# Kernel tuning notes

Hardware: AMD Instinct MI355X
Metric: run time of the kernel (lower is better)

Reference implementation:

```python
import jax, jax.numpy as jnp
import numpy as np

D_MODEL = 512
N_HEADS = 8


def setup_inputs() -> dict:
    key = jax.random.key(0)
    ks = jax.random.split(key, 16)
    bs, S, D = 16, 512, D_MODEL
    def lin(k, fo, fi):
        lim = np.sqrt(6.0 / (fi + fo)).astype(np.float32)
        return jax.random.uniform(k, (fo, fi), jnp.float32, -lim, lim)
    inp = {
        'q': jax.random.normal(ks[0], (bs, S, D), jnp.float32),
        'k': jax.random.normal(ks[1], (bs, S, D), jnp.float32),
        'v': jax.random.normal(ks[2], (bs, S, D), jnp.float32),
        'sgap': jax.random.randint(ks[3], (bs, S), 0, 100, jnp.int64) if jax.config.jax_enable_x64 else jax.random.randint(ks[3], (bs, S), 0, 100, jnp.int32),
        'pcount': jax.random.randint(ks[4], (bs, S), 0, 50, jnp.int32),
        'Wq': lin(ks[5], D, D), 'bq': jnp.zeros((D,), jnp.float32),
        'Wk': lin(ks[6], D, D), 'bk': jnp.zeros((D,), jnp.float32),
        'Wv': lin(ks[7], D, D), 'bv': jnp.zeros((D,), jnp.float32),
        'Wo': lin(ks[8], D, D), 'bo': jnp.zeros((D,), jnp.float32),
        'gammas': jax.random.normal(ks[9], (N_HEADS, 1, 1), jnp.float32) * 0.5,
        'ln_g': jnp.ones((D,), jnp.float32), 'ln_b': jnp.zeros((D,), jnp.float32),
        'Wi1': lin(ks[10], D // 4, 2), 'bi1': jnp.zeros((D // 4,), jnp.float32),
        'Wi2': lin(ks[11], D, D // 4), 'bi2': jnp.zeros((D,), jnp.float32),
        'iscale': jnp.array([0.5], jnp.float32),
    }
    return inp


def reference(q, k, v, sgap, pcount, Wq, bq, Wk, bk, Wv, bv, Wo, bo, gammas, ln_g, ln_b, Wi1, bi1, Wi2, bi2, iscale):
    bs, S, D = q.shape
    h = gammas.shape[0]
    d_k = D // h
    def split_heads(x, W, b):
        return (x @ W.T + b).reshape(bs, S, h, d_k).transpose(0, 2, 1, 3)  # [b,h,S,d]
    qh = split_heads(q, Wq, bq)
    kh = split_heads(k, Wk, bk)
    vh = split_heads(v, Wv, bv)

    scores = jnp.einsum('bhid,bhjd->bhij', qh, kh) / jnp.sqrt(jnp.float32(d_k))
    # strict-causal mask (triu(ones,k=0)==0): attend only to j < i
    mask = jnp.tril(jnp.ones((S, S), bool), k=-1)[None, None]
    NEG = jnp.float32(-1e32)

    # no-grad temporal distance term
    p = jax.nn.softmax(jnp.where(mask, scores, NEG), axis=-1) * mask
    distcum = jnp.cumsum(p, axis=-1)
    disttotal = jnp.sum(p, axis=-1, keepdims=True)
    idx = jnp.arange(S, dtype=jnp.float32)
    pos = jnp.abs(idx[None, :] - idx[:, None])[None, None]
    dist = jax.lax.stop_gradient(jnp.sqrt(jnp.clip((disttotal - distcum) * pos, 0.0, None)))

    gam = -jax.nn.softplus(gammas)[None]  # [1,h,1,1]
    temporal = jnp.clip(jnp.exp(dist * gam), 1e-5, 1e5)
    attn = jax.nn.softmax(jnp.where(mask, scores * temporal, NEG), axis=-1)
    attn = attn.at[:, :, 0, :].set(0.0)  # zero_pad first query position

    X = jnp.einsum('bhij,bhjd->bhid', attn, vh).transpose(0, 2, 1, 3).reshape(bs, S, D)

    # InterferenceAddNorm
    def norm01(x):
        x = x.astype(jnp.float32)
        std = jnp.std(x, ddof=1) + 1e-6
        return (jnp.tanh((x - jnp.mean(x)) / std) + 1.0) / 2.0
    ii = jnp.stack([norm01(sgap), norm01(pcount)], axis=-1)  # [b,S,2]
    feat = jax.nn.relu(ii @ Wi1.T + bi1) @ Wi2.T + bi2
    Y = X + iscale * feat
    mu = jnp.mean(Y, -1, keepdims=True)
    var = jnp.var(Y, -1, keepdims=True)
    Yn = (Y - mu) / jnp.sqrt(var + 1e-5) * ln_g + ln_b
    return Yn @ Wo.T + bo
```

## Files before the change

kernel.cpp:

```cpp
#include <hip/hip_runtime.h>
#include <hip/hip_bf16.h>
#include <math.h>

typedef __attribute__((ext_vector_type(8))) short bf16x8;
typedef __attribute__((ext_vector_type(4))) float f32x4;
typedef __fp16 __attribute__((ext_vector_type(2))) h16x2;

__device__ __forceinline__ f32x4 mfma16(bf16x8 a, bf16x8 b, f32x4 c) {
  return __builtin_amdgcn_mfma_f32_16x16x32_bf16(a, b, c, 0, 0, 0);
}

__device__ __forceinline__ float scan16(float x) {
  int v;
  v = __builtin_amdgcn_update_dpp(0, __float_as_int(x), 0x111, 0xf, 0xf, true);
  x += __int_as_float(v);
  v = __builtin_amdgcn_update_dpp(0, __float_as_int(x), 0x112, 0xf, 0xf, true);
  x += __int_as_float(v);
  v = __builtin_amdgcn_update_dpp(0, __float_as_int(x), 0x114, 0xf, 0xf, true);
  x += __int_as_float(v);
  v = __builtin_amdgcn_update_dpp(0, __float_as_int(x), 0x118, 0xf, 0xf, true);
  x += __int_as_float(v);
  return x;
}

__global__ void stats_kernel(const int* __restrict__ sgap,
                             const int* __restrict__ pcount,
                             float* __restrict__ stats) {
  const int N = 16 * 512;
  long long s0 = 0, q0 = 0, s1 = 0, q1 = 0;
  for (int i = threadIdx.x; i < N; i += 256) {
    long long a = sgap[i];
    long long b = pcount[i];
    s0 += a; q0 += a * a;
    s1 += b; q1 += b * b;
  }
#pragma unroll
  for (int m = 32; m >= 1; m >>= 1) {
    s0 += __shfl_xor(s0, m, 64); q0 += __shfl_xor(q0, m, 64);
    s1 += __shfl_xor(s1, m, 64); q1 += __shfl_xor(q1, m, 64);
  }
  __shared__ long long red[4][4];
  const int w = threadIdx.x >> 6;
  if ((threadIdx.x & 63) == 0) {
    red[w][0] = s0; red[w][1] = q0; red[w][2] = s1; red[w][3] = q1;
  }
  __syncthreads();
  if (threadIdx.x == 0) {
    long long S0 = 0, Q0 = 0, S1 = 0, Q1 = 0;
    for (int i = 0; i < 4; ++i) {
      S0 += red[i][0]; Q0 += red[i][1]; S1 += red[i][2]; Q1 += red[i][3];
    }
    const double n = (double)N;
    const double mean0 = S0 / n, mean1 = S1 / n;
    const double var0 = ((double)Q0 - (double)S0 * (double)S0 / n) / (n - 1.0);
    const double var1 = ((double)Q1 - (double)S1 * (double)S1 / n) / (n - 1.0);
    const float std0 = (float)sqrt(var0) + 1e-6f;
    const float std1 = (float)sqrt(var1) + 1e-6f;
    stats[0] = (float)mean0; stats[1] = 1.0f / std0;
    stats[2] = (float)mean1; stats[3] = 1.0f / std1;
  }
}

template <int AMODE>
__device__ __forceinline__ void gemm_body(const void* __restrict__ Ain,
                                          const float* __restrict__ W,
                                          const float* __restrict__ bias,
                                          void* __restrict__ Out, const int omode) {
  constexpr int LDK = 40;
  __shared__ __hip_bfloat16 As[128 * LDK];
  __shared__ __hip_bfloat16 Bs[128 * LDK];
  const int tid = threadIdx.x;
  const int tm = blockIdx.x * 128;
  const int tn = blockIdx.y * 128;
  const int lane = tid & 63;
  const int wid = tid >> 6;
  const int wm = (wid >> 1) * 64;
  const int wn = (wid & 1) * 64;
  const int g = lane >> 4, l15 = lane & 15;

  const f32x4 Z = {0.f, 0.f, 0.f, 0.f};
  f32x4 acc[4][4];
#pragma unroll
  for (int m = 0; m < 4; ++m)
#pragma unroll
    for (int n = 0; n < 4; ++n) acc[m][n] = Z;

  for (int k0 = 0; k0 < 512; k0 += 32) {
#pragma unroll
    for (int p = 0; p < 4; ++p) {
      const int c = p * 256 + tid;
      const int row = c >> 3;
      const int kc = (c & 7) * 4;
      union { __hip_bfloat16 h[4]; uint2 u; } ua, ub;
      if (AMODE == 0) {
        const float4 x = *(const float4*)((const float*)Ain + (size_t)(tm + row) * 512 + k0 + kc);
        ua.h[0] = __float2bfloat16(x.x); ua.h[1] = __float2bfloat16(x.y);
        ua.h[2] = __float2bfloat16(x.z); ua.h[3] = __float2bfloat16(x.w);
      } else {
        ua.u = *(const uint2*)((const __hip_bfloat16*)Ain + (size_t)(tm + row) * 512 + k0 + kc);
      }
      const float4 wv = *(const float4*)(W + (size_t)(tn + row) * 512 + k0 + kc);
      ub.h[0] = __float2bfloat16(wv.x); ub.h[1] = __float2bfloat16(wv.y);
      ub.h[2] = __float2bfloat16(wv.z); ub.h[3] = __float2bfloat16(wv.w);
      *(uint2*)&As[row * LDK + kc] = ua.u;
      *(uint2*)&Bs[row * LDK + kc] = ub.u;
    }
    __syncthreads();
    bf16x8 af[4], bfv[4];
#pragma unroll
    for (int m = 0; m < 4; ++m)
      af[m] = *(const bf16x8*)&As[(wm + m * 16 + l15) * LDK + g * 8];
#pragma unroll
    for (int n = 0; n < 4; ++n)
      bfv[n] = *(const bf16x8*)&Bs[(wn + n * 16 + l15) * LDK + g * 8];
#pragma unroll
    for (int m = 0; m < 4; ++m)
#pragma unroll
      for (int n = 0; n < 4; ++n)
        acc[m][n] = mfma16(af[m], bfv[n], acc[m][n]);
    __syncthreads();
  }

#pragma unroll
  for (int n = 0; n < 4; ++n) {
    const int cc = tn + wn + n * 16 + l15;
    const float bv = bias[cc];
#pragma unroll
    for (int m = 0; m < 4; ++m) {
#pragma unroll
      for (int jj = 0; jj < 4; ++jj) {
        const int r = tm + wm + m * 16 + g * 4 + jj;
        const float v = acc[m][n][jj] + bv;
        if (omode == 2) {
          ((float*)Out)[(size_t)r * 512 + cc] = v;
        } else {
          const int bb = r >> 9, srow = r & 511, hh = cc >> 6, dd = cc & 63;
          if (omode == 0)
            ((__hip_bfloat16*)Out)[(((size_t)(bb * 8 + hh)) * 512 + srow) * 64 + dd] =
                __float2bfloat16(v);
          else
            ((__hip_bfloat16*)Out)[(((size_t)(bb * 8 + hh)) * 64 + dd) * 512 + srow] =
                __float2bfloat16(v);
        }
      }
    }
  }
}

__global__ __launch_bounds__(256) void gemm_qkv(
    const float* __restrict__ q, const float* __restrict__ k,
    const float* __restrict__ v, const float* __restrict__ Wq,
    const float* __restrict__ bq, const float* __restrict__ Wk,
    const float* __restrict__ bk, const float* __restrict__ Wv,
    const float* __restrict__ bv, __hip_bfloat16* __restrict__ qh,
    __hip_bfloat16* __restrict__ kh, __hip_bfloat16* __restrict__ vhT) {
  const int z = blockIdx.z;
  const float* A = (z == 0) ? q : (z == 1) ? k : v;
  const float* W = (z == 0) ? Wq : (z == 1) ? Wk : Wv;
  const float* bias = (z == 0) ? bq : (z == 1) ? bk : bv;
  void* Out = (z == 0) ? (void*)qh : (z == 1) ? (void*)kh : (void*)vhT;
  gemm_body<0>(A, W, bias, Out, (z == 2) ? 1 : 0);
}

__global__ __launch_bounds__(256) void gemm_wo(const __hip_bfloat16* __restrict__ Yn,
                                               const float* __restrict__ Wo,
                                               const float* __restrict__ bo,
                                               float* __restrict__ Out) {
  gemm_body<1>(Yn, Wo, bo, Out, 2);
}

#define PLD 40

__device__ __forceinline__ void attn_unit(
    const __hip_bfloat16* __restrict__ Q, const __hip_bfloat16* __restrict__ K,
    const __hip_bfloat16* __restrict__ V, __hip_bfloat16* __restrict__ Xb,
    __hip_bfloat16* Pw, const int i0, const int ntile, const float gam,
    const int b, const int h, const int lane) {
  const int g = lane >> 4, l15 = lane & 15;
  const float scale = 0.125f;
  const f32x4 Z = {0.f, 0.f, 0.f, 0.f};

  const bf16x8 qf0 = *(const bf16x8*)&Q[(i0 + l15) * 64 + g * 8];
  const bf16x8 qf1 = *(const bf16x8*)&Q[(i0 + l15) * 64 + 32 + g * 8];

  h16x2 sp[64];
  float d1p[4] = {0.f, 0.f, 0.f, 0.f};
#pragma unroll
  for (int t = 0; t < 32; ++t) {
    if (t < ntile) {
      const bf16x8 kf0 = *(const bf16x8*)&K[(t * 16 + l15) * 64 + g * 8];
      const bf16x8 kf1 = *(const bf16x8*)&K[(t * 16 + l15) * 64 + 32 + g * 8];
      f32x4 s = mfma16(qf0, kf0, Z);
      s = mfma16(qf1, kf1, s);
      sp[2 * t] = __builtin_amdgcn_cvt_pkrtz(s[0] * scale, s[1] * scale);
      sp[2 * t + 1] = __builtin_amdgcn_cvt_pkrtz(s[2] * scale, s[3] * scale);
      const int j = t * 16 + l15;
#pragma unroll
      for (int jj = 0; jj < 4; ++jj) {
        const float sv = (float)((jj < 2) ? sp[2 * t][jj] : sp[2 * t + 1][jj - 2]);
        const int i = i0 + g * 4 + jj;
        d1p[jj] += (j < i) ? __expf(sv) : 0.f;
      }
    }
  }
  float invd1[4];
#pragma unroll
  for (int jj = 0; jj < 4; ++jj) {
    float dd = d1p[jj];
#pragma unroll
    for (int m = 8; m >= 1; m >>= 1) dd += __shfl_xor(dd, m, 16);
    invd1[jj] = dd > 0.f ? 1.f / dd : 0.f;
  }

  f32x4 accx[4] = {Z, Z, Z, Z};
  float carry[4] = {0.f, 0.f, 0.f, 0.f};
  float d2p[4] = {0.f, 0.f, 0.f, 0.f};

#pragma unroll
  for (int tp = 0; tp < 16; ++tp) {
    if (tp * 2 < ntile) {
      __hip_bfloat16* Pb = Pw + (tp & 1) * (16 * PLD);
#pragma unroll
      for (int half = 0; half < 2; ++half) {
        const int t = tp * 2 + half;
        float e2v[4] = {0.f, 0.f, 0.f, 0.f};
        if (t < ntile) {
          const int j = t * 16 + l15;
#pragma unroll
          for (int jj = 0; jj < 4; ++jj) {
            const float sv = (float)((jj < 2) ? sp[2 * t][jj] : sp[2 * t + 1][jj - 2]);
            const int i = i0 + g * 4 + jj;
            const bool valid = j < i;
            const float p = valid ? __expf(sv) * invd1[jj] : 0.f;
            const float cs = scan16(p) + carry[jj];
            const float suffix = 1.f - cs;
            carry[jj] = __shfl(cs, 15, 16);
            const float dist = sqrtf(fmaxf(suffix * (float)(i - j), 0.f));
            const float tempo = fmaxf(__expf(gam * dist), 1e-5f);
            const float e2 = valid ? __expf(sv * tempo) : 0.f;
            d2p[jj] += e2;
            e2v[jj] = e2;
          }
        }
#pragma unroll
        for (int jj = 0; jj < 4; ++jj)
          Pb[(g * 4 + jj) * PLD + half * 16 + l15] = __float2bfloat16(e2v[jj]);
      }
      asm volatile("s_waitcnt lgkmcnt(0)" ::: "memory");
      const bf16x8 pf = *(const bf16x8*)&Pb[l15 * PLD + g * 8];
#pragma unroll
      for (int n = 0; n < 4; ++n) {
        const bf16x8 vf =
            *(const bf16x8*)&V[(size_t)(n * 16 + l15) * 512 + tp * 32 + g * 8];
        accx[n] = mfma16(pf, vf, accx[n]);
      }
    }
  }

#pragma unroll
  for (int jj = 0; jj < 4; ++jj) {
    float dd = d2p[jj];
#pragma unroll
    for (int m = 8; m >= 1; m >>= 1) dd += __shfl_xor(dd, m, 16);
    d2p[jj] = dd > 0.f ? 1.f / dd : 0.f;
  }
#pragma unroll
  for (int n = 0; n < 4; ++n) {
#pragma unroll
    for (int jj = 0; jj < 4; ++jj) {
      const int i = i0 + g * 4 + jj;
      const float val = (i > 0) ? accx[n][jj] * d2p[jj] : 0.f;
      Xb[((size_t)(b * 512 + i)) * 512 + h * 64 + n * 16 + l15] = __float2bfloat16(val);
    }
  }
}

__global__ __launch_bounds__(64) void attn_kernel(
    const __hip_bfloat16* __restrict__ qh, const __hip_bfloat16* __restrict__ kh,
    const __hip_bfloat16* __restrict__ vhT, const float* __restrict__ gammas,
    __hip_bfloat16* __restrict__ Xb) {
  __shared__ __hip_bfloat16 Psh[2 * 16 * PLD];
  const int lane = threadIdx.x;
  const int work = (blockIdx.x & 7) * 256 + (blockIdx.x >> 3);
  const int bh = work >> 4;
  const int pr = work & 15;
  const int b = bh >> 3, h = bh & 7;

  const __hip_bfloat16* Q = qh + (size_t)bh * (512 * 64);
  const __hip_bfloat16* K = kh + (size_t)bh * (512 * 64);
  const __hip_bfloat16* V = vhT + (size_t)bh * (64 * 512);
  const float gam = -log1pf(expf(gammas[h]));

  attn_unit(Q, K, V, Xb, Psh, pr * 16, pr + 1, gam, b, h, lane);
  attn_unit(Q, K, V, Xb, Psh, (31 - pr) * 16, 32 - pr, gam, b, h, lane);
}

__global__ __launch_bounds__(256) void addnorm_kernel(
    const __hip_bfloat16* __restrict__ Xb, const int* __restrict__ sgap,
    const int* __restrict__ pcount, const float* __restrict__ stats,
    const float* __restrict__ Wi1, const float* __restrict__ bi1,
    const float* __restrict__ Wi2, const float* __restrict__ bi2,
    const float* __restrict__ iscale, const float* __restrict__ ln_g,
    const float* __restrict__ ln_b, __hip_bfloat16* __restrict__ Yn) {
  constexpr int WLD = 132;
  __shared__ __hip_bfloat16 Wt[256 * WLD];
  __shared__ __hip_bfloat16 Hs[64 * WLD];
  __shared__ float iis[64][2];
  __shared__ float red[4][64][2];
  const int tid = threadIdx.x;
  const int lane = tid & 63;
  const int w = tid >> 6;
  const int g = lane >> 4, l15 = lane & 15;
  const int t0 = blockIdx.x * 64;

  if (tid < 64) {
    const float a0 = ((float)sgap[t0 + tid] - stats[0]) * stats[1];
    const float a1 = ((float)pcount[t0 + tid] - stats[2]) * stats[3];
    iis[tid][0] = (tanhf(a0) + 1.f) * 0.5f;
    iis[tid][1] = (tanhf(a1) + 1.f) * 0.5f;
  }
  __syncthreads();

  {
    const int tt = tid & 63;
    const int jb = w * 32;
    const float a = iis[tt][0], b = iis[tt][1];
#pragma unroll
    for (int jj = 0; jj < 32; ++jj) {
      const int j = jb + jj;
      const float hv = fmaxf(Wi1[j * 2] * a + Wi1[j * 2 + 1] * b + bi1[j], 0.f);
      Hs[tt * WLD + j] = __float2bfloat16(hv);
    }
  }

  const f32x4 Z = {0.f, 0.f, 0.f, 0.f};
  f32x4 acc[4][8];
#pragma unroll
  for (int m = 0; m < 4; ++m)
#pragma unroll
    for (int n = 0; n < 8; ++n) acc[m][n] = Z;

  for (int half = 0; half < 2; ++half) {
    if (half) __syncthreads();
#pragma unroll
    for (int p = 0; p < 32; ++p) {
      const int idx = p * 256 + tid;
      const int r = idx >> 5;
      const int c4 = (idx & 31) * 4;
      const float4 x = *(const float4*)(Wi2 + ((size_t)(half * 256 + r)) * 128 + c4);
      union { __hip_bfloat16 h[4]; uint2 u; } ub;
      ub.h[0] = __float2bfloat16(x.x); ub.h[1] = __float2bfloat16(x.y);
      ub.h[2] = __float2bfloat16(x.z); ub.h[3] = __float2bfloat16(x.w);
      *(uint2*)&Wt[r * WLD + c4] = ub.u;
    }
    __syncthreads();
#pragma unroll
    for (int k = 0; k < 4; ++k) {
      bf16x8 af[4];
#pragma unroll
      for (int m = 0; m < 4; ++m)
        af[m] = *(const bf16x8*)&Hs[(m * 16 + l15) * WLD + k * 32 + g * 8];
#pragma unroll
      for (int n = 0; n < 4; ++n) {
        const bf16x8 bf =
            *(const bf16x8*)&Wt[(w * 64 + n * 16 + l15) * WLD + k * 32 + g * 8];
#pragma unroll
        for (int m = 0; m < 4; ++m)
          acc[m][half * 4 + n] = mfma16(af[m], bf, acc[m][half * 4 + n]);
      }
    }
  }

  const float sc = iscale[0];
  float bi[8], lg[8], lb[8];
#pragma unroll
  for (int nn = 0; nn < 8; ++nn) {
    const int c = (nn >> 2) * 256 + w * 64 + (nn & 3) * 16 + l15;
    bi[nn] = bi2[c]; lg[nn] = ln_g[c]; lb[nn] = ln_b[c];
  }

#pragma unroll
  for (int m = 0; m < 4; ++m) {
#pragma unroll
    for (int jj = 0; jj < 4; ++jj) {
      const int r = m * 16 + g * 4 + jj;
      float s = 0.f, sq = 0.f;
#pragma unroll
      for (int nn = 0; nn < 8; ++nn) {
        const int c = (nn >> 2) * 256 + w * 64 + (nn & 3) * 16 + l15;
        const float fv = acc[m][nn][jj] + bi[nn];
        const float y =
            __bfloat162float(Xb[(size_t)(t0 + r) * 512 + c]) + sc * fv;
        acc[m][nn][jj] = y;
        s += y; sq += y * y;
      }
#pragma unroll
      for (int mk = 8; mk >= 1; mk >>= 1) {
        s += __shfl_xor(s, mk, 16);
        sq += __shfl_xor(sq, mk, 16);
      }
      if (l15 == 0) { red[w][r][0] = s; red[w][r][1] = sq; }
    }
  }
  __syncthreads();

#pragma unroll
  for (int m = 0; m < 4; ++m) {
#pragma unroll
    for (int jj = 0; jj < 4; ++jj) {
      const int r = m * 16 + g * 4 + jj;
      const float sum = red[0][r][0] + red[1][r][0] + red[2][r][0] + red[3][r][0];
      const float sqs = red[0][r][1] + red[1][r][1] + red[2][r][1] + red[3][r][1];
      const float mu = sum * (1.f / 512.f);
      const float var = sqs * (1.f / 512.f) - mu * mu;
      const float rstd = rsqrtf(var + 1e-5f);
#pragma unroll
      for (int nn = 0; nn < 8; ++nn) {
        const int c = (nn >> 2) * 256 + w * 64 + (nn & 3) * 16 + l15;
        Yn[(size_t)(t0 + r) * 512 + c] =
            __float2bfloat16((acc[m][nn][jj] - mu) * rstd * lg[nn] + lb[nn]);
      }
    }
  }
}

extern "C" void kernel_launch(void* const* d_in, const int* in_sizes, int n_in,
                              void* d_out, int out_size, void* d_ws, size_t ws_size,
                              hipStream_t stream) {
  const float* q = (const float*)d_in[0];
  const float* k = (const float*)d_in[1];
  const float* v = (const float*)d_in[2];
  const int* sgap = (const int*)d_in[3];
  const int* pcount = (const int*)d_in[4];
  const float* Wq = (const float*)d_in[5];
  const float* bq = (const float*)d_in[6];
  const float* Wk = (const float*)d_in[7];
  const float* bk = (const float*)d_in[8];
  const float* Wv = (const float*)d_in[9];
  const float* bv = (const float*)d_in[10];
  const float* Wo = (const float*)d_in[11];
  const float* bo = (const float*)d_in[12];
  const float* gammas = (const float*)d_in[13];
  const float* ln_g = (const float*)d_in[14];
  const float* ln_b = (const float*)d_in[15];
  const float* Wi1 = (const float*)d_in[16];
  const float* bi1 = (const float*)d_in[17];
  const float* Wi2 = (const float*)d_in[18];
  const float* bi2 = (const float*)d_in[19];
  const float* iscale = (const float*)d_in[20];

  char* ws = (char*)d_ws;
  __hip_bfloat16* qh = (__hip_bfloat16*)(ws);
  __hip_bfloat16* kh = (__hip_bfloat16*)(ws + ((size_t)8 << 20));
  __hip_bfloat16* vhT = (__hip_bfloat16*)(ws + ((size_t)16 << 20));
  __hip_bfloat16* Xb = (__hip_bfloat16*)(ws + ((size_t)24 << 20));
  __hip_bfloat16* Yn = (__hip_bfloat16*)(ws + ((size_t)32 << 20));
  float* stats = (float*)(ws + ((size_t)40 << 20));

  stats_kernel<<<1, 256, 0, stream>>>(sgap, pcount, stats);
  gemm_qkv<<<dim3(64, 4, 3), 256, 0, stream>>>(q, k, v, Wq, bq, Wk, bk, Wv, bv,
                                               qh, kh, vhT);
  attn_kernel<<<2048, 64, 0, stream>>>(qh, kh, vhT, gammas, Xb);
  addnorm_kernel<<<128, 256, 0, stream>>>(Xb, sgap, pcount, stats, Wi1, bi1, Wi2,
                                          bi2, iscale, ln_g, ln_b, Yn);
  gemm_wo<<<dim3(64, 4), 256, 0, stream>>>(Yn, Wo, bo, (float*)d_out);
}
```

Measured before the change: 265.8 us.

## Shrink tiles and per-block work to launch more blocks across all kernels

The shared GEMM body moves from 128x128 to 128x64 tiles, so the QKV and output projections launch twice as many blocks. The attention kernel stops pairing a short and a long row-group per block and gives each block one row-group, with a launch-bounds occupancy hint. The add-norm kernel handles 16 tokens per block instead of 64 and reads Wi2 straight from global memory rather than staging it in LDS. The goal is better CU fill and latency hiding, at the cost of more repeated A-tile and weight loads and uneven causal work across attention blocks.

```diff
diff --git a/kernel.cpp b/kernel.cpp
--- a/kernel.cpp
+++ b/kernel.cpp
@@ -68,20 +68,19 @@
                                           void* __restrict__ Out, const int omode) {
   constexpr int LDK = 40;
   __shared__ __hip_bfloat16 As[128 * LDK];
-  __shared__ __hip_bfloat16 Bs[128 * LDK];
+  __shared__ __hip_bfloat16 Bs[64 * LDK];
   const int tid = threadIdx.x;
   const int tm = blockIdx.x * 128;
-  const int tn = blockIdx.y * 128;
+  const int tn = blockIdx.y * 64;
   const int lane = tid & 63;
   const int wid = tid >> 6;
-  const int wm = (wid >> 1) * 64;
-  const int wn = (wid & 1) * 64;
+  const int wm = wid * 32;
   const int g = lane >> 4, l15 = lane & 15;
 
   const f32x4 Z = {0.f, 0.f, 0.f, 0.f};
-  f32x4 acc[4][4];
-#pragma unroll
-  for (int m = 0; m < 4; ++m)
+  f32x4 acc[2][4];
+#pragma unroll
+  for (int m = 0; m < 2; ++m)
 #pragma unroll
     for (int n = 0; n < 4; ++n) acc[m][n] = Z;
 
@@ -91,7 +90,7 @@
       const int c = p * 256 + tid;
       const int row = c >> 3;
       const int kc = (c & 7) * 4;
-      union { __hip_bfloat16 h[4]; uint2 u; } ua, ub;
+      union { __hip_bfloat16 h[4]; uint2 u; } ua;
       if (AMODE == 0) {
         const float4 x = *(const float4*)((const float*)Ain + (size_t)(tm + row) * 512 + k0 + kc);
         ua.h[0] = __float2bfloat16(x.x); ua.h[1] = __float2bfloat16(x.y);
@@ -99,22 +98,25 @@
       } else {
         ua.u = *(const uint2*)((const __hip_bfloat16*)Ain + (size_t)(tm + row) * 512 + k0 + kc);
       }
-      const float4 wv = *(const float4*)(W + (size_t)(tn + row) * 512 + k0 + kc);
-      ub.h[0] = __float2bfloat16(wv.x); ub.h[1] = __float2bfloat16(wv.y);
-      ub.h[2] = __float2bfloat16(wv.z); ub.h[3] = __float2bfloat16(wv.w);
       *(uint2*)&As[row * LDK + kc] = ua.u;
-      *(uint2*)&Bs[row * LDK + kc] = ub.u;
+      if (p < 2) {
+        union { __hip_bfloat16 h[4]; uint2 u; } ub;
+        const float4 wv = *(const float4*)(W + (size_t)(tn + row) * 512 + k0 + kc);
+        ub.h[0] = __float2bfloat16(wv.x); ub.h[1] = __float2bfloat16(wv.y);
+        ub.h[2] = __float2bfloat16(wv.z); ub.h[3] = __float2bfloat16(wv.w);
+        *(uint2*)&Bs[row * LDK + kc] = ub.u;
+      }
     }
     __syncthreads();
-    bf16x8 af[4], bfv[4];
-#pragma unroll
-    for (int m = 0; m < 4; ++m)
+    bf16x8 af[2], bfv[4];
+#pragma unroll
+    for (int m = 0; m < 2; ++m)
       af[m] = *(const bf16x8*)&As[(wm + m * 16 + l15) * LDK + g * 8];
 #pragma unroll
     for (int n = 0; n < 4; ++n)
-      bfv[n] = *(const bf16x8*)&Bs[(wn + n * 16 + l15) * LDK + g * 8];
-#pragma unroll
-    for (int m = 0; m < 4; ++m)
+      bfv[n] = *(const bf16x8*)&Bs[(n * 16 + l15) * LDK + g * 8];
+#pragma unroll
+    for (int m = 0; m < 2; ++m)
 #pragma unroll
       for (int n = 0; n < 4; ++n)
         acc[m][n] = mfma16(af[m], bfv[n], acc[m][n]);
@@ -123,10 +125,10 @@
 
 #pragma unroll
   for (int n = 0; n < 4; ++n) {
-    const int cc = tn + wn + n * 16 + l15;
+    const int cc = tn + n * 16 + l15;
     const float bv = bias[cc];
 #pragma unroll
-    for (int m = 0; m < 4; ++m) {
+    for (int m = 0; m < 2; ++m) {
 #pragma unroll
       for (int jj = 0; jj < 4; ++jj) {
         const int r = tm + wm + m * 16 + g * 4 + jj;
@@ -275,15 +277,15 @@
   }
 }
 
-__global__ __launch_bounds__(64) void attn_kernel(
+__global__ __launch_bounds__(64, 4) void attn_kernel(
     const __hip_bfloat16* __restrict__ qh, const __hip_bfloat16* __restrict__ kh,
     const __hip_bfloat16* __restrict__ vhT, const float* __restrict__ gammas,
     __hip_bfloat16* __restrict__ Xb) {
   __shared__ __hip_bfloat16 Psh[2 * 16 * PLD];
   const int lane = threadIdx.x;
-  const int work = (blockIdx.x & 7) * 256 + (blockIdx.x >> 3);
-  const int bh = work >> 4;
-  const int pr = work & 15;
+  const int work = (blockIdx.x & 7) * 512 + (blockIdx.x >> 3);
+  const int bh = work >> 5;
+  const int rg = work & 31;
   const int b = bh >> 3, h = bh & 7;
 
   const __hip_bfloat16* Q = qh + (size_t)bh * (512 * 64);
@@ -291,8 +293,7 @@
   const __hip_bfloat16* V = vhT + (size_t)bh * (64 * 512);
   const float gam = -log1pf(expf(gammas[h]));
 
-  attn_unit(Q, K, V, Xb, Psh, pr * 16, pr + 1, gam, b, h, lane);
-  attn_unit(Q, K, V, Xb, Psh, (31 - pr) * 16, 32 - pr, gam, b, h, lane);
+  attn_unit(Q, K, V, Xb, Psh, rg * 16, rg + 1, gam, b, h, lane);
 }
 
 __global__ __launch_bounds__(256) void addnorm_kernel(
@@ -303,17 +304,16 @@
     const float* __restrict__ iscale, const float* __restrict__ ln_g,
     const float* __restrict__ ln_b, __hip_bfloat16* __restrict__ Yn) {
   constexpr int WLD = 132;
-  __shared__ __hip_bfloat16 Wt[256 * WLD];
-  __shared__ __hip_bfloat16 Hs[64 * WLD];
-  __shared__ float iis[64][2];
-  __shared__ float red[4][64][2];
+  __shared__ __hip_bfloat16 Hs[16 * WLD];
+  __shared__ float iis[16][2];
+  __shared__ float red[4][16][2];
   const int tid = threadIdx.x;
   const int lane = tid & 63;
   const int w = tid >> 6;
   const int g = lane >> 4, l15 = lane & 15;
-  const int t0 = blockIdx.x * 64;
-
-  if (tid < 64) {
+  const int t0 = blockIdx.x * 16;
+
+  if (tid < 16) {
     const float a0 = ((float)sgap[t0 + tid] - stats[0]) * stats[1];
     const float a1 = ((float)pcount[t0 + tid] - stats[2]) * stats[3];
     iis[tid][0] = (tanhf(a0) + 1.f) * 0.5f;
@@ -322,52 +322,37 @@
   __syncthreads();
 
   {
-    const int tt = tid & 63;
-    const int jb = w * 32;
+    const int tt = tid & 15;
+    const int jb = (tid >> 4) * 8;
     const float a = iis[tt][0], b = iis[tt][1];
 #pragma unroll
-    for (int jj = 0; jj < 32; ++jj) {
+    for (int jj = 0; jj < 8; ++jj) {
       const int j = jb + jj;
       const float hv = fmaxf(Wi1[j * 2] * a + Wi1[j * 2 + 1] * b + bi1[j], 0.f);
       Hs[tt * WLD + j] = __float2bfloat16(hv);
     }
   }
+  __syncthreads();
 
   const f32x4 Z = {0.f, 0.f, 0.f, 0.f};
-  f32x4 acc[4][8];
-#pragma unroll
-  for (int m = 0; m < 4; ++m)
-#pragma unroll
-    for (int n = 0; n < 8; ++n) acc[m][n] = Z;
-
-  for (int half = 0; half < 2; ++half) {
-    if (half) __syncthreads();
-#pragma unroll
-    for (int p = 0; p < 32; ++p) {
-      const int idx = p * 256 + tid;
-      const int r = idx >> 5;
-      const int c4 = (idx & 31) * 4;
-      const float4 x = *(const float4*)(Wi2 + ((size_t)(half * 256 + r)) * 128 + c4);
-      union { __hip_bfloat16 h[4]; uint2 u; } ub;
-      ub.h[0] = __float2bfloat16(x.x); ub.h[1] = __float2bfloat16(x.y);
-      ub.h[2] = __float2bfloat16(x.z); ub.h[3] = __float2bfloat16(x.w);
-      *(uint2*)&Wt[r * WLD + c4] = ub.u;
-    }
-    __syncthreads();
-#pragma unroll
-    for (int k = 0; k < 4; ++k) {
-      bf16x8 af[4];
-#pragma unroll
-      for (int m = 0; m < 4; ++m)
-        af[m] = *(const bf16x8*)&Hs[(m * 16 + l15) * WLD + k * 32 + g * 8];
-#pragma unroll
-      for (int n = 0; n < 4; ++n) {
-        const bf16x8 bf =
-            *(const bf16x8*)&Wt[(w * 64 + n * 16 + l15) * WLD + k * 32 + g * 8];
-#pragma unroll
-        for (int m = 0; m < 4; ++m)
-          acc[m][half * 4 + n] = mfma16(af[m], bf, acc[m][half * 4 + n]);
-      }
+  f32x4 acc[8];
+#pragma unroll
+  for (int n = 0; n < 8; ++n) acc[n] = Z;
+
+#pragma unroll
+  for (int k = 0; k < 4; ++k) {
+    const bf16x8 af = *(const bf16x8*)&Hs[l15 * WLD + k * 32 + g * 8];
+#pragma unroll
+    for (int n = 0; n < 8; ++n) {
+      const int col = w * 128 + n * 16 + l15;
+      const float4 x0 = *(const float4*)(Wi2 + (size_t)col * 128 + k * 32 + g * 8);
+      const float4 x1 = *(const float4*)(Wi2 + (size_t)col * 128 + k * 32 + g * 8 + 4);
+      union { __hip_bfloat16 hh[8]; bf16x8 v8; } ub;
+      ub.hh[0] = __float2bfloat16(x0.x); ub.hh[1] = __float2bfloat16(x0.y);
+      ub.hh[2] = __float2bfloat16(x0.z); ub.hh[3] = __float2bfloat16(x0.w);
+      ub.hh[4] = __float2bfloat16(x1.x); ub.hh[5] = __float2bfloat16(x1.y);
+      ub.hh[6] = __float2bfloat16(x1.z); ub.hh[7] = __float2bfloat16(x1.w);
+      acc[n] = mfma16(af, ub.v8, acc[n]);
     }
   }
 
@@ -375,51 +360,44 @@
   float bi[8], lg[8], lb[8];
 #pragma unroll
   for (int nn = 0; nn < 8; ++nn) {
-    const int c = (nn >> 2) * 256 + w * 64 + (nn & 3) * 16 + l15;
+    const int c = w * 128 + nn * 16 + l15;
     bi[nn] = bi2[c]; lg[nn] = ln_g[c]; lb[nn] = ln_b[c];
   }
 
 #pragma unroll
-  for (int m = 0; m < 4; ++m) {
-#pragma unroll
-    for (int jj = 0; jj < 4; ++jj) {
-      const int r = m * 16 + g * 4 + jj;
-      float s = 0.f, sq = 0.f;
-#pragma unroll
-      for (int nn = 0; nn < 8; ++nn) {
-        const int c = (nn >> 2) * 256 + w * 64 + (nn & 3) * 16 + l15;
-        const float fv = acc[m][nn][jj] + bi[nn];
-        const float y =
-            __bfloat162float(Xb[(size_t)(t0 + r) * 512 + c]) + sc * fv;
-        acc[m][nn][jj] = y;
-        s += y; sq += y * y;
-      }
-#pragma unroll
-      for (int mk = 8; mk >= 1; mk >>= 1) {
-        s += __shfl_xor(s, mk, 16);
-        sq += __shfl_xor(sq, mk, 16);
-      }
-      if (l15 == 0) { red[w][r][0] = s; red[w][r][1] = sq; }
-    }
+  for (int jj = 0; jj < 4; ++jj) {
+    const int r = g * 4 + jj;
+    float s = 0.f, sq = 0.f;
+#pragma unroll
+    for (int nn = 0; nn < 8; ++nn) {
+      const int c = w * 128 + nn * 16 + l15;
+      const float fv = acc[nn][jj] + bi[nn];
+      const float y = __bfloat162float(Xb[(size_t)(t0 + r) * 512 + c]) + sc * fv;
+      acc[nn][jj] = y;
+      s += y; sq += y * y;
+    }
+#pragma unroll
+    for (int mk = 8; mk >= 1; mk >>= 1) {
+      s += __shfl_xor(s, mk, 16);
+      sq += __shfl_xor(sq, mk, 16);
+    }
+    if (l15 == 0) { red[w][r][0] = s; red[w][r][1] = sq; }
   }
   __syncthreads();
 
 #pragma unroll
-  for (int m = 0; m < 4; ++m) {
-#pragma unroll
-    for (int jj = 0; jj < 4; ++jj) {
-      const int r = m * 16 + g * 4 + jj;
-      const float sum = red[0][r][0] + red[1][r][0] + red[2][r][0] + red[3][r][0];
-      const float sqs = red[0][r][1] + red[1][r][1] + red[2][r][1] + red[3][r][1];
-      const float mu = sum * (1.f / 512.f);
-      const float var = sqs * (1.f / 512.f) - mu * mu;
-      const float rstd = rsqrtf(var + 1e-5f);
-#pragma unroll
-      for (int nn = 0; nn < 8; ++nn) {
-        const int c = (nn >> 2) * 256 + w * 64 + (nn & 3) * 16 + l15;
-        Yn[(size_t)(t0 + r) * 512 + c] =
-            __float2bfloat16((acc[m][nn][jj] - mu) * rstd * lg[nn] + lb[nn]);
-      }
+  for (int jj = 0; jj < 4; ++jj) {
+    const int r = g * 4 + jj;
+    const float sum = red[0][r][0] + red[1][r][0] + red[2][r][0] + red[3][r][0];
+    const float sqs = red[0][r][1] + red[1][r][1] + red[2][r][1] + red[3][r][1];
+    const float mu = sum * (1.f / 512.f);
+    const float var = sqs * (1.f / 512.f) - mu * mu;
+    const float rstd = rsqrtf(var + 1e-5f);
+#pragma unroll
+    for (int nn = 0; nn < 8; ++nn) {
+      const int c = w * 128 + nn * 16 + l15;
+      Yn[(size_t)(t0 + r) * 512 + c] =
+          __float2bfloat16((acc[nn][jj] - mu) * rstd * lg[nn] + lb[nn]);
     }
   }
 }
@@ -458,10 +436,10 @@
   float* stats = (float*)(ws + ((size_t)40 << 20));
 
   stats_kernel<<<1, 256, 0, stream>>>(sgap, pcount, stats);
-  gemm_qkv<<<dim3(64, 4, 3), 256, 0, stream>>>(q, k, v, Wq, bq, Wk, bk, Wv, bv,
+  gemm_qkv<<<dim3(64, 8, 3), 256, 0, stream>>>(q, k, v, Wq, bq, Wk, bk, Wv, bv,
                                                qh, kh, vhT);
-  attn_kernel<<<2048, 64, 0, stream>>>(qh, kh, vhT, gammas, Xb);
-  addnorm_kernel<<<128, 256, 0, stream>>>(Xb, sgap, pcount, stats, Wi1, bi1, Wi2,
+  attn_kernel<<<4096, 64, 0, stream>>>(qh, kh, vhT, gammas, Xb);
+  addnorm_kernel<<<512, 256, 0, stream>>>(Xb, sgap, pcount, stats, Wi1, bi1, Wi2,
                                           bi2, iscale, ln_g, ln_b, Yn);
-  gemm_wo<<<dim3(64, 4), 256, 0, stream>>>(Yn, Wo, bo, (float*)d_out);
-}
+  gemm_wo<<<dim3(64, 8), 256, 0, stream>>>(Yn, Wo, bo, (float*)d_out);
+}
```

After: 293.4 us. +10.4%, slower.
